# Kernel tuning notes

Hardware: AMD Instinct MI355X
Metric: run time of the kernel (lower is better)

The kernel has to match this reference:

```python
import jax, jax.numpy as jnp
import numpy as np

DIM = 32          # d_model == channel dim of the volume
D_STATE = 16
D_CONV = 4
EXPAND = 2
D_INNER = EXPAND * DIM        # 64
DT_RANK = max(1, (DIM + 15) // 16)  # ceil(d_model/16) = 2
LN_EPS = 1e-5


def setup_inputs() -> dict:
    key = jax.random.key(0)
    ks = jax.random.split(key, 12)
    B, Dd, Hh, Ww = 1, 32, 32, 32
    sc = 0.02
    x = jax.random.normal(ks[0], (B, DIM, Dd, Hh, Ww), jnp.float32)
    ln_w = jnp.ones((DIM,), jnp.float32)
    ln_b = jnp.zeros((DIM,), jnp.float32)
    in_proj_w = jax.random.normal(ks[1], (2 * D_INNER, DIM), jnp.float32) * sc
    conv_w = jax.random.normal(ks[2], (D_INNER, 1, D_CONV), jnp.float32) * sc
    conv_b = jnp.zeros((D_INNER,), jnp.float32)
    x_proj_w = jax.random.normal(ks[3], (DT_RANK + 2 * D_STATE, D_INNER), jnp.float32) * sc
    dt_proj_w = jax.random.normal(ks[4], (D_INNER, DT_RANK), jnp.float32) * sc
    dt_proj_b = jax.random.uniform(ks[5], (D_INNER,), jnp.float32, -4.0, -2.0)  # small softplus(dt) at init
    # Mamba S4D-real init: A = -[1..d_state], stored as A_log
    A_log = jnp.log(jnp.broadcast_to(jnp.arange(1, D_STATE + 1, dtype=jnp.float32), (D_INNER, D_STATE)))
    D_param = jnp.ones((D_INNER,), jnp.float32)
    out_proj_w = jax.random.normal(ks[6], (DIM, D_INNER), jnp.float32) * sc
    return {
        "x": x, "ln_w": ln_w, "ln_b": ln_b, "in_proj_w": in_proj_w,
        "conv_w": conv_w, "conv_b": conv_b, "x_proj_w": x_proj_w,
        "dt_proj_w": dt_proj_w, "dt_proj_b": dt_proj_b, "A_log": A_log,
        "D_param": D_param, "out_proj_w": out_proj_w,
    }


def _mamba_layer(x, ln_w, ln_b, in_proj_w, conv_w, conv_b, x_proj_w,
                 dt_proj_w, dt_proj_b, A_log, D_param, out_proj_w):
    B, C, Dd, Hh, Ww = x.shape
    L = Dd * Hh * Ww
    # z-scan flatten: (B, C, D, H, W) -> (B, L, C)
    xf = x.reshape(B, C, L).transpose(0, 2, 1)
    # LayerNorm over channel dim
    mu = jnp.mean(xf, axis=-1, keepdims=True)
    var = jnp.mean(jnp.square(xf - mu), axis=-1, keepdims=True)
    xn = (xf - mu) * jax.lax.rsqrt(var + LN_EPS) * ln_w + ln_b
    # in_proj -> x, z branches
    xz = xn @ in_proj_w.T                      # (B, L, 2*d_inner)
    x_in, z = jnp.split(xz, 2, axis=-1)
    # depthwise causal conv1d over sequence
    xt = x_in.transpose(0, 2, 1)               # (B, d_inner, L)
    xc = jax.lax.conv_general_dilated(
        xt, conv_w, window_strides=(1,), padding=[(D_CONV - 1, 0)],
        feature_group_count=D_INNER)
    xc = jax.nn.silu(xc + conv_b[None, :, None]).transpose(0, 2, 1)  # (B, L, d_inner)
    # input-dependent dt, B, C
    x_dbl = xc @ x_proj_w.T                    # (B, L, dt_rank + 2*d_state)
    dt, Bm, Cm = jnp.split(x_dbl, [DT_RANK, DT_RANK + D_STATE], axis=-1)
    delta = jax.nn.softplus(dt @ dt_proj_w.T + dt_proj_b)            # (B, L, d_inner)
    A = -jnp.exp(A_log)                        # (d_inner, d_state)
    # discretize: h_t = exp(delta*A) h_{t-1} + delta*B_t*x_t
    dA = jnp.exp(delta[..., None] * A)                               # (B, L, d_inner, d_state)
    dBx = delta[..., None] * Bm[:, :, None, :] * xc[..., None]       # (B, L, d_inner, d_state)
    def comb(e1, e2):
        a1, b1 = e1
        a2, b2 = e2
        return (a1 * a2, a2 * b1 + b2)
    _, h = jax.lax.associative_scan(comb, (dA, dBx), axis=1)         # parallel linear recurrence
    y = jnp.einsum('blds,bls->bld', h, Cm) + xc * D_param            # (B, L, d_inner)
    y = y * jax.nn.silu(z)
    out = y @ out_proj_w.T                     # (B, L, C)
    # unpermute z-scan
    return out.transpose(0, 2, 1).reshape(B, C, Dd, Hh, Ww)


def reference(x, ln_w, ln_b, in_proj_w, conv_w, conv_b, x_proj_w,
              dt_proj_w, dt_proj_b, A_log, D_param, out_proj_w):
    return _mamba_layer(x, ln_w, ln_b, in_proj_w, conv_w, conv_b, x_proj_w,
                        dt_proj_w, dt_proj_b, A_log, D_param, out_proj_w)
```

## Files before the change

### kernel.cpp

```cpp
#include <hip/hip_runtime.h>
#include <hip/hip_bf16.h>

constexpr int L   = 32768;
constexpr int CD  = 32;
constexpr int DI  = 64;
constexpr int DS  = 16;
constexpr int LC  = 32;
constexpr int NCH = L / LC;
constexpr int NPAIR = DI * DS;

constexpr size_t FL        = (size_t)DI * L;
constexpr size_t OFF_XC    = 0;
constexpr size_t OFF_DELTA = FL;
constexpr size_t OFF_BM    = 2 * FL;
constexpr size_t OFF_CM    = OFF_BM + (size_t)DS * L;
constexpr size_t OFF_APROD = OFF_CM + (size_t)DS * L;
constexpr size_t OFF_CARRY = OFF_APROD;
constexpr size_t OFF_BACC  = OFF_APROD + (size_t)NCH * NPAIR;

__device__ __forceinline__ float bf2f(__hip_bfloat16 v) { return __bfloat162float(v); }

__device__ __forceinline__ bool detect_bf16(const void* ln_w) {
    return ((const unsigned short*)ln_w)[0] == 0x3F80;
}
__device__ __forceinline__ float ldin(const void* p, size_t i, bool bf16) {
    return bf16 ? bf2f(((const __hip_bfloat16*)p)[i]) : ((const float*)p)[i];
}

__device__ __forceinline__ float dot32_g(const void* w, int row, const float* xv, bool isb) {
    float acc = 0.f;
    if (isb) {
        const __hip_bfloat16* p = (const __hip_bfloat16*)w + (size_t)row * 32;
        #pragma unroll
        for (int c = 0; c < 32; ++c) acc += bf2f(p[c]) * xv[c];
    } else {
        const float4* p = (const float4*)((const float*)w + (size_t)row * 32);
        #pragma unroll
        for (int q = 0; q < 8; ++q) {
            const float4 w4 = p[q];
            acc += w4.x * xv[4*q] + w4.y * xv[4*q+1] + w4.z * xv[4*q+2] + w4.w * xv[4*q+3];
        }
    }
    return acc;
}

__global__ __launch_bounds__(256) void k12_featurize_scan(
    const void* __restrict__ x,
    const void* __restrict__ ln_w,
    const void* __restrict__ ln_b,
    const void* __restrict__ in_proj_w,
    const void* __restrict__ conv_w,
    const void* __restrict__ conv_b,
    const void* __restrict__ x_proj_w,
    const void* __restrict__ dt_proj_w,
    const void* __restrict__ dt_proj_b,
    const void* __restrict__ A_log,
    float* __restrict__ ws)
{
    __shared__ __align__(16) char smem[33040];
    float (*xin_s)[36]  = (float(*)[36])(smem);
    float (*sxc)[36]    = (float(*)[36])(smem);
    char* AR = smem + 9216;
    float (*xn_s)[33]   = (float(*)[33])(AR);
    float (*w_in_s)[32] = (float(*)[32])(AR + 4624);
    float (*sdl)[36]    = (float(*)[36])(AR);
    float (*sbm)[36]    = (float(*)[36])(AR + 9216);
    char* FW = smem + 22032;
    float (*w_xp)[64]   = (float(*)[64])(FW);
    float (*w_cv)[4]    = (float(*)[4])(FW + 8704);
    float (*w_dt)[2]    = (float(*)[2])(FW + 9728);
    float* b_dt_s = (float*)(FW + 10240);
    float* b_cv_s = (float*)(FW + 10496);
    float* lnw_s  = (float*)(FW + 10752);
    float* lnb_s  = (float*)(FW + 10880);

    const int tid = threadIdx.x;
    const int l0  = blockIdx.x * LC;
    const bool isb = detect_bf16(ln_w);

    if (isb) {
        const __hip_bfloat16* ipw = (const __hip_bfloat16*)in_proj_w;
        const __hip_bfloat16* xpw = (const __hip_bfloat16*)x_proj_w;
        for (int i = tid; i < 64 * 32; i += 256) ((float*)w_in_s)[i] = bf2f(ipw[i]);
        for (int i = tid; i < 34 * 64; i += 256) ((float*)w_xp)[i] = bf2f(xpw[i]);
    } else {
        const float4* ipw = (const float4*)in_proj_w;
        const float4* xpw = (const float4*)x_proj_w;
        #pragma unroll
        for (int k = 0; k < 2; ++k) ((float4*)w_in_s)[tid + 256 * k] = ipw[tid + 256 * k];
        for (int i = tid; i < 544; i += 256) ((float4*)w_xp)[i] = xpw[i];
    }
    w_cv[tid >> 2][tid & 3] = ldin(conv_w, tid, isb);
    if (tid < 128) w_dt[tid >> 1][tid & 1] = ldin(dt_proj_w, tid, isb);
    if (tid < 64) { b_dt_s[tid] = ldin(dt_proj_b, tid, isb); b_cv_s[tid] = ldin(conv_b, tid, isb); }
    if (tid < 32) { lnw_s[tid] = ldin(ln_w, tid, isb); lnb_s[tid] = ldin(ln_b, tid, isb); }
    __syncthreads();

    if (tid < LC + 3) {
        const int l = l0 - 3 + tid;
        const bool valid = (l >= 0);
        const int lc = valid ? l : 0;
        float xv[CD];
        if (isb) {
            const __hip_bfloat16* xb = (const __hip_bfloat16*)x;
            #pragma unroll
            for (int c = 0; c < CD; ++c) xv[c] = bf2f(xb[(size_t)c * L + lc]);
        } else {
            const float* xf = (const float*)x;
            #pragma unroll
            for (int c = 0; c < CD; ++c) xv[c] = xf[(size_t)c * L + lc];
        }
        float mu = 0.f;
        #pragma unroll
        for (int c = 0; c < CD; ++c) mu += xv[c];
        mu *= (1.f / CD);
        float var = 0.f;
        #pragma unroll
        for (int c = 0; c < CD; ++c) { const float dc = xv[c] - mu; var += dc * dc; }
        const float rstd = rsqrtf(var * (1.f / CD) + 1e-5f);
        #pragma unroll
        for (int c = 0; c < CD; ++c)
            xn_s[tid][c] = valid ? ((xv[c] - mu) * rstd * lnw_s[c] + lnb_s[c]) : 0.f;
    }
    __syncthreads();

    {
        const int colq = tid & 31;
        const int rgrp = tid >> 5;
        float xv[CD];
        #pragma unroll
        for (int c = 0; c < CD; ++c) xv[c] = xn_s[colq][c];
        #pragma unroll
        for (int j = 0; j < 8; ++j) {
            const int row = rgrp * 8 + j;
            const float4* wr = (const float4*)w_in_s[row];
            float a0 = 0.f;
            #pragma unroll
            for (int q = 0; q < 8; ++q) {
                const float4 w4 = wr[q];
                a0 += w4.x * xv[4*q] + w4.y * xv[4*q+1] + w4.z * xv[4*q+2] + w4.w * xv[4*q+3];
            }
            xin_s[row][colq] = a0;
        }
        if (tid < 192) {
            const int row = tid & 63;
            const int cH  = 32 + (tid >> 6);
            float xvh[CD];
            #pragma unroll
            for (int c = 0; c < CD; ++c) xvh[c] = xn_s[cH][c];
            xin_s[row][cH] = dot32_g(in_proj_w, row, xvh, isb);
        }
    }
    __syncthreads();

    {
        const int h  = tid & 7;
        const int pq = tid >> 3;
        const int l  = l0 + pq;
        const int dbase = h * 8;
        float xcv[8];
        #pragma unroll
        for (int i = 0; i < 8; ++i) {
            const int d = dbase + i;
            float acc = b_cv_s[d];
            #pragma unroll
            for (int k = 0; k < 4; ++k) acc += w_cv[d][k] * xin_s[d][pq + k];
            const float v = acc / (1.f + __expf(-acc));
            xcv[i] = v;
            ws[OFF_XC + (size_t)d * L + l] = v;
        }
        float dt0 = 0.f, dt1 = 0.f;
        for (int r = 0; r < 34; ++r) {
            float acc = 0.f;
            #pragma unroll
            for (int i = 0; i < 8; ++i) acc += w_xp[r][dbase + i] * xcv[i];
            acc += __shfl_xor(acc, 1);
            acc += __shfl_xor(acc, 2);
            acc += __shfl_xor(acc, 4);
            if (r == 0) dt0 = acc;
            else if (r == 1) dt1 = acc;
            else {
                const int rr = r - 2;
                if (h == (rr >> 2)) {
                    const size_t off = (rr < 16) ? (OFF_BM + (size_t)rr * L)
                                                 : (OFF_CM + (size_t)(rr - 16) * L);
                    ws[off + l] = acc;
                    if (rr < 16) sbm[rr][pq] = acc;
                }
            }
        }
        #pragma unroll
        for (int i = 0; i < 8; ++i) {
            const int d = dbase + i;
            const float tv = dt0 * w_dt[d][0] + dt1 * w_dt[d][1] + b_dt_s[d];
            const float sp = fmaxf(tv, 0.f) + log1pf(__expf(-fabsf(tv)));
            ws[OFF_DELTA + (size_t)d * L + l] = sp;
            sdl[d][pq] = sp;
        }
        __syncthreads();
        #pragma unroll
        for (int i = 0; i < 8; ++i) sxc[dbase + i][pq] = xcv[i];
    }
    __syncthreads();

    {
        const int d = tid >> 2, sg = tid & 3;
        float Aj[4], ap[4] = {1.f, 1.f, 1.f, 1.f}, bb[4] = {0.f, 0.f, 0.f, 0.f};
        #pragma unroll
        for (int j = 0; j < 4; ++j) Aj[j] = -__expf(ldin(A_log, d * DS + sg + 4 * j, isb));

        auto cstep = [&](float dd, float xx, int col) {
            const float dxc = dd * xx;
            #pragma unroll
            for (int j = 0; j < 4; ++j) {
                const float e = __expf(dd * Aj[j]);
                ap[j] *= e;
                bb[j] = e * bb[j] + dxc * sbm[sg + 4 * j][col];
            }
        };
        for (int t = 0; t < LC; t += 4) {
            const float4 dd4 = *(const float4*)&sdl[d][t];
            const float4 xx4 = *(const float4*)&sxc[d][t];
            cstep(dd4.x, xx4.x, t);
            cstep(dd4.y, xx4.y, t + 1);
            cstep(dd4.z, xx4.z, t + 2);
            cstep(dd4.w, xx4.w, t + 3);
        }
        *(float4*)&ws[OFF_APROD + (size_t)blockIdx.x * NPAIR + tid * 4] = make_float4(ap[0], ap[1], ap[2], ap[3]);
        *(float4*)&ws[OFF_BACC  + (size_t)blockIdx.x * NPAIR + tid * 4] = make_float4(bb[0], bb[1], bb[2], bb[3]);
    }
}

__global__ __launch_bounds__(256) void k3_carry(float* __restrict__ ws)
{
    __shared__ float ctile[4][NCH];
    const int lane = threadIdx.x & 63;
    const int wv   = threadIdx.x >> 6;
    const int bid  = blockIdx.x;
    const int pg   = ((bid & 7) << 5) | (bid >> 3);
    const int p    = pg * 4 + wv;

    float a[16], b[16];
    #pragma unroll
    for (int i = 0; i < 16; ++i) {
        const size_t ch = (size_t)(lane * 16 + i);
        a[i] = ws[OFF_APROD + ch * NPAIR + p];
        b[i] = ws[OFF_BACC  + ch * NPAIR + p];
    }

    float Ag = a[0], Bg = b[0];
    #pragma unroll
    for (int i = 1; i < 16; ++i) { Bg = a[i] * Bg + b[i]; Ag = Ag * a[i]; }
    #pragma unroll
    for (int off = 1; off < 64; off <<= 1) {
        const float pa = __shfl_up(Ag, off);
        const float pb = __shfl_up(Bg, off);
        if (lane >= off) { Bg = Ag * pb + Bg; Ag = Ag * pa; }
    }
    float Pb = __shfl_up(Bg, 1);
    if (lane == 0) Pb = 0.f;
    #pragma unroll
    for (int i = 0; i < 16; ++i) { ctile[wv][lane * 16 + i] = Pb; Pb = a[i] * Pb + b[i]; }
    __syncthreads();
    #pragma unroll
    for (int r = 0; r < 4; ++r) {
        const int ch = threadIdx.x + 256 * r;
        *(float4*)&ws[OFF_CARRY + (size_t)ch * NPAIR + pg * 4] =
            make_float4(ctile[0][ch], ctile[1][ch], ctile[2][ch], ctile[3][ch]);
    }
}

__global__ __launch_bounds__(256) void k45_apply_out(
    const void* __restrict__ x,
    const void* __restrict__ ln_w,
    const void* __restrict__ ln_b,
    const void* __restrict__ in_proj_w,
    const void* __restrict__ A_log,
    const void* __restrict__ D_param,
    const void* __restrict__ out_proj_w,
    float* __restrict__ ws,
    void* __restrict__ out)
{
    __shared__ __align__(16) char smem45[26880];
    float (*sx)[36]      = (float(*)[36])(smem45);
    float (*sy)[36]      = (float(*)[36])(smem45 + 4608);
    float (*sbm)[36]     = (float(*)[36])(smem45 + 13824);
    float (*scm)[36]     = (float(*)[36])(smem45 + 16128);
    float (*w_out_s)[64] = (float(*)[64])(smem45 + 18432);
    float* lnw_s = (float*)(smem45 + 26624);
    float* lnb_s = (float*)(smem45 + 26752);

    const int tid = threadIdx.x;
    const int c   = blockIdx.x;
    const size_t t0 = (size_t)c * LC;
    const bool isb = detect_bf16(ln_w);

    {
        const int r = tid >> 3, t4 = (tid & 7) * 4;
        if (isb) {
            const __hip_bfloat16* xb = (const __hip_bfloat16*)x;
            #pragma unroll
            for (int k = 0; k < 4; ++k) sx[r][t4 + k] = bf2f(xb[(size_t)r * L + t0 + t4 + k]);
        } else {
            *(float4*)&sx[r][t4] = *(const float4*)&((const float*)x)[(size_t)r * L + t0 + t4];
        }
    }
    {
        const int q = tid & 127;
        const int r = q >> 3, t4 = (q & 7) * 4;
        const size_t src = ((tid < 128) ? OFF_BM : OFF_CM) + (size_t)r * L + t0 + t4;
        float* dst = (tid < 128) ? &sbm[r][t4] : &scm[r][t4];
        *(float4*)dst = *(const float4*)&ws[src];
    }
    if (isb) {
        const __hip_bfloat16* opw = (const __hip_bfloat16*)out_proj_w;
        for (int i = tid; i < CD * DI; i += 256) ((float*)w_out_s)[i] = bf2f(opw[i]);
    } else {
        const float4* opw = (const float4*)out_proj_w;
        #pragma unroll
        for (int k = 0; k < 2; ++k) ((float4*)w_out_s)[tid + 256 * k] = opw[tid + 256 * k];
    }
    if (tid < 32) { lnw_s[tid] = ldin(ln_w, tid, isb); lnb_s[tid] = ldin(ln_b, tid, isb); }
    __syncthreads();

    {
        const int pos  = tid & 31;
        const int rgrp = tid >> 5;
        float xnv[CD];
        #pragma unroll
        for (int ch = 0; ch < CD; ++ch) xnv[ch] = sx[ch][pos];
        float mu = 0.f;
        #pragma unroll
        for (int ch = 0; ch < CD; ++ch) mu += xnv[ch];
        mu *= (1.f / CD);
        float var = 0.f;
        #pragma unroll
        for (int ch = 0; ch < CD; ++ch) { const float dc = xnv[ch] - mu; var += dc * dc; }
        const float rstd = rsqrtf(var * (1.f / CD) + 1e-5f);
        #pragma unroll
        for (int ch = 0; ch < CD; ++ch) xnv[ch] = (xnv[ch] - mu) * rstd * lnw_s[ch] + lnb_s[ch];
        #pragma unroll
        for (int j = 0; j < 8; ++j) {
            const int row = 64 + rgrp * 8 + j;
            const float acc = dot32_g(in_proj_w, row, xnv, isb);
            sy[rgrp * 8 + j][pos] = acc / (1.f + __expf(-acc));
        }
    }
    __syncthreads();

    {
        const int d = tid >> 2, sg = tid & 3;
        float Aj[4];
        #pragma unroll
        for (int j = 0; j < 4; ++j) Aj[j] = -__expf(ldin(A_log, d * DS + sg + 4 * j, isb));
        const float Dd = ldin(D_param, d, isb);
        float hh[4];
        {
            const float4 h4 = *(const float4*)&ws[OFF_CARRY + (size_t)c * NPAIR + tid * 4];
            hh[0] = h4.x; hh[1] = h4.y; hh[2] = h4.z; hh[3] = h4.w;
        }
        const float* dlp = ws + OFF_DELTA + (size_t)d * L + t0;
        const float* xcp = ws + OFF_XC    + (size_t)d * L + t0;

        auto step = [&](float dd, float xx, int col) {
            const float dxc = dd * xx;
            float ys = 0.f;
            #pragma unroll
            for (int j = 0; j < 4; ++j) {
                const float e = __expf(dd * Aj[j]);
                hh[j] = e * hh[j] + dxc * sbm[sg + 4 * j][col];
                ys += hh[j] * scm[sg + 4 * j][col];
            }
            ys += __shfl_xor(ys, 1);
            ys += __shfl_xor(ys, 2);
            if (sg == 0) sy[d][col] *= (ys + xx * Dd);
        };
        for (int t = 0; t < LC; t += 4) {
            const float4 dd4 = *(const float4*)(dlp + t);
            const float4 xx4 = *(const float4*)(xcp + t);
            step(dd4.x, xx4.x, t);
            step(dd4.y, xx4.y, t + 1);
            step(dd4.z, xx4.z, t + 2);
            step(dd4.w, xx4.w, t + 3);
        }
    }
    __syncthreads();

    {
        const int wv   = tid >> 6;
        const int lane = tid & 63;
        const int pos  = lane & 31;
        const int cg   = lane >> 5;
        float acc[4] = {0.f, 0.f, 0.f, 0.f};
        for (int dd = 0; dd < DI; ++dd) {
            const float yv = sy[dd][pos];
            #pragma unroll
            for (int j = 0; j < 4; ++j)
                acc[j] += yv * w_out_s[wv * 8 + cg * 4 + j][dd];
        }
        const size_t l = t0 + pos;
        #pragma unroll
        for (int j = 0; j < 4; ++j) {
            const int cc = wv * 8 + cg * 4 + j;
            if (isb) ((__hip_bfloat16*)out)[(size_t)cc * L + l] = __float2bfloat16(acc[j]);
            else     ((float*)out)[(size_t)cc * L + l] = acc[j];
        }
    }
}

extern "C" void kernel_launch(void* const* d_in, const int* in_sizes, int n_in,
                              void* d_out, int out_size, void* d_ws, size_t ws_size,
                              hipStream_t stream)
{
    (void)in_sizes; (void)n_in; (void)out_size; (void)ws_size;
    const void* x        = d_in[0];
    const void* ln_w     = d_in[1];
    const void* ln_b     = d_in[2];
    const void* in_pw    = d_in[3];
    const void* conv_w   = d_in[4];
    const void* conv_b   = d_in[5];
    const void* x_pw     = d_in[6];
    const void* dt_pw    = d_in[7];
    const void* dt_pb    = d_in[8];
    const void* A_log    = d_in[9];
    const void* D_param  = d_in[10];
    const void* out_pw   = d_in[11];
    float* ws = (float*)d_ws;

    k12_featurize_scan<<<NCH, 256, 0, stream>>>(x, ln_w, ln_b, in_pw, conv_w, conv_b,
                                                x_pw, dt_pw, dt_pb, A_log, ws);
    k3_carry<<<NPAIR / 4, 256, 0, stream>>>(ws);
    k45_apply_out<<<NCH, 256, 0, stream>>>(x, ln_w, ln_b, in_pw, A_log, D_param,
                                           out_pw, ws, d_out);
}
```

Measured before the change: 181.4 us.

## Split LayerNorm across lanes, stage z-weights in LDS, cap registers for occupancy

Both kernels now declare launch bounds asking for two blocks per CU, which caps register use. In k12 the LayerNorm is spread over four lanes per position with shuffle reductions instead of one thread holding 32 values, and one projection loop is only partly unrolled. In k45 the z-branch weights are staged in shared memory and LayerNorm stats are computed once per position, while out_proj weights are read straight from global (cache) instead of LDS. These cut register pressure and per-thread serial work, at the cost of extra syncs, shuffles and uncached-in-LDS global weight loads in the inner output loop.

```diff
diff --git a/kernel.cpp b/kernel.cpp
--- a/kernel.cpp
+++ b/kernel.cpp
@@ -44,7 +44,7 @@
     return acc;
 }
 
-__global__ __launch_bounds__(256) void k12_featurize_scan(
+__global__ __launch_bounds__(256, 2) void k12_featurize_scan(
     const void* __restrict__ x,
     const void* __restrict__ ln_w,
     const void* __restrict__ ln_b,
@@ -96,31 +96,32 @@
     if (tid < 32) { lnw_s[tid] = ldin(ln_w, tid, isb); lnb_s[tid] = ldin(ln_b, tid, isb); }
     __syncthreads();
 
-    if (tid < LC + 3) {
-        const int l = l0 - 3 + tid;
+    if (tid < 140) {
+        const int pos = tid >> 2;
+        const int q   = tid & 3;
+        const int l = l0 - 3 + pos;
         const bool valid = (l >= 0);
         const int lc = valid ? l : 0;
-        float xv[CD];
-        if (isb) {
-            const __hip_bfloat16* xb = (const __hip_bfloat16*)x;
-            #pragma unroll
-            for (int c = 0; c < CD; ++c) xv[c] = bf2f(xb[(size_t)c * L + lc]);
-        } else {
-            const float* xf = (const float*)x;
-            #pragma unroll
-            for (int c = 0; c < CD; ++c) xv[c] = xf[(size_t)c * L + lc];
-        }
-        float mu = 0.f;
-        #pragma unroll
-        for (int c = 0; c < CD; ++c) mu += xv[c];
-        mu *= (1.f / CD);
-        float var = 0.f;
-        #pragma unroll
-        for (int c = 0; c < CD; ++c) { const float dc = xv[c] - mu; var += dc * dc; }
-        const float rstd = rsqrtf(var * (1.f / CD) + 1e-5f);
-        #pragma unroll
-        for (int c = 0; c < CD; ++c)
-            xn_s[tid][c] = valid ? ((xv[c] - mu) * rstd * lnw_s[c] + lnb_s[c]) : 0.f;
+        float xq[8];
+        #pragma unroll
+        for (int i = 0; i < 8; ++i) xq[i] = ldin(x, (size_t)(q * 8 + i) * L + lc, isb);
+        float s = 0.f;
+        #pragma unroll
+        for (int i = 0; i < 8; ++i) s += xq[i];
+        s += __shfl_xor(s, 1);
+        s += __shfl_xor(s, 2);
+        const float mu = s * (1.f / CD);
+        float d2 = 0.f;
+        #pragma unroll
+        for (int i = 0; i < 8; ++i) { const float dc = xq[i] - mu; d2 += dc * dc; }
+        d2 += __shfl_xor(d2, 1);
+        d2 += __shfl_xor(d2, 2);
+        const float rstd = rsqrtf(d2 * (1.f / CD) + 1e-5f);
+        #pragma unroll
+        for (int i = 0; i < 8; ++i) {
+            const int ch = q * 8 + i;
+            xn_s[pos][ch] = valid ? ((xq[i] - mu) * rstd * lnw_s[ch] + lnb_s[ch]) : 0.f;
+        }
     }
     __syncthreads();
 
@@ -130,7 +131,7 @@
         float xv[CD];
         #pragma unroll
         for (int c = 0; c < CD; ++c) xv[c] = xn_s[colq][c];
-        #pragma unroll
+        #pragma unroll 2
         for (int j = 0; j < 8; ++j) {
             const int row = rgrp * 8 + j;
             const float4* wr = (const float4*)w_in_s[row];
@@ -270,7 +271,7 @@
     }
 }
 
-__global__ __launch_bounds__(256) void k45_apply_out(
+__global__ __launch_bounds__(256, 2) void k45_apply_out(
     const void* __restrict__ x,
     const void* __restrict__ ln_w,
     const void* __restrict__ ln_b,
@@ -281,14 +282,16 @@
     float* __restrict__ ws,
     void* __restrict__ out)
 {
-    __shared__ __align__(16) char smem45[26880];
-    float (*sx)[36]      = (float(*)[36])(smem45);
-    float (*sy)[36]      = (float(*)[36])(smem45 + 4608);
-    float (*sbm)[36]     = (float(*)[36])(smem45 + 13824);
-    float (*scm)[36]     = (float(*)[36])(smem45 + 16128);
-    float (*w_out_s)[64] = (float(*)[64])(smem45 + 18432);
-    float* lnw_s = (float*)(smem45 + 26624);
-    float* lnb_s = (float*)(smem45 + 26752);
+    __shared__ __align__(16) char smem45[27392];
+    float (*sx)[36]  = (float(*)[36])(smem45);
+    float (*sy)[36]  = (float(*)[36])(smem45 + 4608);
+    float (*sbm)[36] = (float(*)[36])(smem45 + 13824);
+    float (*scm)[36] = (float(*)[36])(smem45 + 16128);
+    float (*w_z)[33] = (float(*)[33])(smem45 + 18432);
+    float* lnw_s = (float*)(smem45 + 26880);
+    float* lnb_s = (float*)(smem45 + 27008);
+    float* mu_s  = (float*)(smem45 + 27136);
+    float* rs_s  = (float*)(smem45 + 27264);
 
     const int tid = threadIdx.x;
     const int c   = blockIdx.x;
@@ -312,39 +315,45 @@
         float* dst = (tid < 128) ? &sbm[r][t4] : &scm[r][t4];
         *(float4*)dst = *(const float4*)&ws[src];
     }
-    if (isb) {
-        const __hip_bfloat16* opw = (const __hip_bfloat16*)out_proj_w;
-        for (int i = tid; i < CD * DI; i += 256) ((float*)w_out_s)[i] = bf2f(opw[i]);
-    } else {
-        const float4* opw = (const float4*)out_proj_w;
-        #pragma unroll
-        for (int k = 0; k < 2; ++k) ((float4*)w_out_s)[tid + 256 * k] = opw[tid + 256 * k];
+    #pragma unroll
+    for (int k = 0; k < 8; ++k) {
+        const int idx = tid + 256 * k;
+        w_z[idx >> 5][idx & 31] = ldin(in_proj_w, (size_t)(64 << 5) + idx, isb);
     }
     if (tid < 32) { lnw_s[tid] = ldin(ln_w, tid, isb); lnb_s[tid] = ldin(ln_b, tid, isb); }
+    __syncthreads();
+
+    if (tid < 128) {
+        const int pos = tid >> 2;
+        const int q   = tid & 3;
+        float s = 0.f;
+        #pragma unroll
+        for (int i = 0; i < 8; ++i) s += sx[q * 8 + i][pos];
+        s += __shfl_xor(s, 1);
+        s += __shfl_xor(s, 2);
+        const float mu = s * (1.f / CD);
+        float d2 = 0.f;
+        #pragma unroll
+        for (int i = 0; i < 8; ++i) { const float dc = sx[q * 8 + i][pos] - mu; d2 += dc * dc; }
+        d2 += __shfl_xor(d2, 1);
+        d2 += __shfl_xor(d2, 2);
+        if (q == 0) { mu_s[pos] = mu; rs_s[pos] = rsqrtf(d2 * (1.f / CD) + 1e-5f); }
+    }
     __syncthreads();
 
     {
         const int pos  = tid & 31;
         const int rgrp = tid >> 5;
-        float xnv[CD];
-        #pragma unroll
-        for (int ch = 0; ch < CD; ++ch) xnv[ch] = sx[ch][pos];
-        float mu = 0.f;
-        #pragma unroll
-        for (int ch = 0; ch < CD; ++ch) mu += xnv[ch];
-        mu *= (1.f / CD);
-        float var = 0.f;
-        #pragma unroll
-        for (int ch = 0; ch < CD; ++ch) { const float dc = xnv[ch] - mu; var += dc * dc; }
-        const float rstd = rsqrtf(var * (1.f / CD) + 1e-5f);
-        #pragma unroll
-        for (int ch = 0; ch < CD; ++ch) xnv[ch] = (xnv[ch] - mu) * rstd * lnw_s[ch] + lnb_s[ch];
-        #pragma unroll
-        for (int j = 0; j < 8; ++j) {
-            const int row = 64 + rgrp * 8 + j;
-            const float acc = dot32_g(in_proj_w, row, xnv, isb);
-            sy[rgrp * 8 + j][pos] = acc / (1.f + __expf(-acc));
-        }
+        const float mu = mu_s[pos], rstd = rs_s[pos];
+        float acc[8] = {0.f, 0.f, 0.f, 0.f, 0.f, 0.f, 0.f, 0.f};
+        for (int ch = 0; ch < CD; ++ch) {
+            const float xnc = (sx[ch][pos] - mu) * rstd * lnw_s[ch] + lnb_s[ch];
+            #pragma unroll
+            for (int j = 0; j < 8; ++j) acc[j] += xnc * w_z[rgrp * 8 + j][ch];
+        }
+        #pragma unroll
+        for (int j = 0; j < 8; ++j)
+            sy[rgrp * 8 + j][pos] = acc[j] / (1.f + __expf(-acc[j]));
     }
     __syncthreads();
 
@@ -391,17 +400,29 @@
         const int lane = tid & 63;
         const int pos  = lane & 31;
         const int cg   = lane >> 5;
+        const int c0   = wv * 8 + cg * 4;
         float acc[4] = {0.f, 0.f, 0.f, 0.f};
-        for (int dd = 0; dd < DI; ++dd) {
-            const float yv = sy[dd][pos];
-            #pragma unroll
-            for (int j = 0; j < 4; ++j)
-                acc[j] += yv * w_out_s[wv * 8 + cg * 4 + j][dd];
+        if (isb) {
+            const __hip_bfloat16* opw = (const __hip_bfloat16*)out_proj_w;
+            for (int dd = 0; dd < DI; ++dd) {
+                const float yv = sy[dd][pos];
+                #pragma unroll
+                for (int j = 0; j < 4; ++j)
+                    acc[j] += yv * bf2f(opw[(size_t)(c0 + j) * DI + dd]);
+            }
+        } else {
+            const float* opw = (const float*)out_proj_w;
+            for (int dd = 0; dd < DI; ++dd) {
+                const float yv = sy[dd][pos];
+                #pragma unroll
+                for (int j = 0; j < 4; ++j)
+                    acc[j] += yv * opw[(size_t)(c0 + j) * DI + dd];
+            }
         }
         const size_t l = t0 + pos;
         #pragma unroll
         for (int j = 0; j < 4; ++j) {
-            const int cc = wv * 8 + cg * 4 + j;
+            const int cc = c0 + j;
             if (isb) ((__hip_bfloat16*)out)[(size_t)cc * L + l] = __float2bfloat16(acc[j]);
             else     ((float*)out)[(size_t)cc * L + l] = acc[j];
         }
```

Measured after the change: 157.0 us. -13.5%, faster.
